# Performance work log

Measured on AMD Instinct MI355X. Metric: run time of the kernel, lower is better.

Reference implementation:

```python
import jax, jax.numpy as jnp
import numpy as np

D = 768
LAYERS = 4
LN_EPS = 1e-5


def _layer_norm(h, g, b):
    m = jnp.mean(h, axis=-1, keepdims=True)
    v = jnp.var(h, axis=-1, keepdims=True)
    return (h - m) * jax.lax.rsqrt(v + LN_EPS) * g + b


def _encode(ids, emb, ln_g, ln_b, w1, b1, w2, b2):
    # ids: [N, F] int, emb: [F, V, D] stacked embedding tables
    h = emb[0][ids[:, 0]]
    for i in range(1, emb.shape[0]):
        h = h + emb[i][ids[:, i]]
    h = _layer_norm(h, ln_g, ln_b)
    h = jax.nn.gelu(jnp.dot(h, w1) + b1)
    return jnp.dot(h, w2) + b2


def setup_inputs() -> dict:
    key = jax.random.key(0)
    ks = jax.random.split(key, 24)
    N, E = 50000, 100000
    s = 0.02
    inp = {
        "x": jax.random.randint(ks[0], (N, 9), 0, 128),
        "edge_attr": jax.random.randint(ks[1], (E, 3), 0, 8),
        "edge_index": jax.random.randint(ks[2], (2, E), 0, N),
        # AtomEncoder params
        "atom_emb": jax.random.normal(ks[3], (9, 128, D), jnp.float32) * s,
        "atom_ln_g": jnp.ones((D,), jnp.float32),
        "atom_ln_b": jnp.zeros((D,), jnp.float32),
        "atom_w1": jax.random.normal(ks[4], (D, D), jnp.float32) * s,
        "atom_b1": jnp.zeros((D,), jnp.float32),
        "atom_w2": jax.random.normal(ks[5], (D, D), jnp.float32) * s,
        "atom_b2": jnp.zeros((D,), jnp.float32),
        # BondEncoder params
        "bond_emb": jax.random.normal(ks[6], (3, 8, D), jnp.float32) * s,
        "bond_ln_g": jnp.ones((D,), jnp.float32),
        "bond_ln_b": jnp.zeros((D,), jnp.float32),
        "bond_w1": jax.random.normal(ks[7], (D, D), jnp.float32) * s,
        "bond_b1": jnp.zeros((D,), jnp.float32),
        "bond_w2": jax.random.normal(ks[8], (D, D), jnp.float32) * s,
        "bond_b2": jnp.zeros((D,), jnp.float32),
        # Per-layer GINEConv MLPs + LayerNorms (stacked over layers)
        "conv_w1": jax.random.normal(ks[9], (LAYERS, D, D), jnp.float32) * s,
        "conv_b1": jnp.zeros((LAYERS, D), jnp.float32),
        "conv_w2": jax.random.normal(ks[10], (LAYERS, D, D), jnp.float32) * s,
        "conv_b2": jnp.zeros((LAYERS, D), jnp.float32),
        "ln_g": jnp.ones((LAYERS, D), jnp.float32),
        "ln_b": jnp.zeros((LAYERS, D), jnp.float32),
    }
    return inp


def reference(x, edge_attr, edge_index,
              atom_emb, atom_ln_g, atom_ln_b, atom_w1, atom_b1, atom_w2, atom_b2,
              bond_emb, bond_ln_g, bond_ln_b, bond_w1, bond_b1, bond_w2, bond_b2,
              conv_w1, conv_b1, conv_w2, conv_b2, ln_g, ln_b):
    N = x.shape[0]
    src, dst = edge_index[0], edge_index[1]
    h = _encode(x, atom_emb, atom_ln_g, atom_ln_b, atom_w1, atom_b1, atom_w2, atom_b2)
    e = _encode(edge_attr, bond_emb, bond_ln_g, bond_ln_b, bond_w1, bond_b1, bond_w2, bond_b2)
    for l in range(LAYERS):
        h_in = h
        # GINEConv (eps=0): out = MLP(x + sum_{j in N(i)} relu(x_j + e_ij))
        msg = jax.nn.relu(h[src] + e)                       # [E, D] gather + edge-add + relu
        agg = jax.ops.segment_sum(msg, dst, num_segments=N)  # scatter-add to nodes
        z = h + agg
        z = jnp.dot(jax.nn.relu(jnp.dot(z, conv_w1[l]) + conv_b1[l]), conv_w2[l]) + conv_b2[l]
        # gelu -> dropout (identity at eval) -> residual LayerNorm
        h = _layer_norm(jax.nn.gelu(z) + h_in, ln_g[l], ln_b[l])
    return h
```

## Files before the change

kernel.cpp:

```cpp
#include <hip/hip_runtime.h>


#define DM 768
#define NLAYERS 4
#define CHUNK 50048

typedef _Float16 f16;
typedef __attribute__((ext_vector_type(8))) _Float16 f16x8;
typedef __attribute__((ext_vector_type(4))) _Float16 f16x4;
typedef __attribute__((ext_vector_type(4))) float f32x4;

__device__ __forceinline__ float gelu_f(float x) {
    float x3 = x * x * x;
    return 0.5f * x * (1.0f + tanhf(0.7978845608028654f * (x + 0.044715f * x3)));
}
__device__ __forceinline__ void async16(const void* g, void* l) {
    __builtin_amdgcn_global_load_lds((const __attribute__((address_space(1))) void*)g,
                                     (__attribute__((address_space(3))) void*)l,
                                     16, 0, 0);
}

__device__ __forceinline__ int xcd_swizzle(int b, int nb) {
    int xcd = b & 7;
    int pos = b >> 3;
    int q = nb >> 3, r = nb & 7;
    int base = (xcd < r) ? xcd * (q + 1) : r * (q + 1) + (xcd - r) * q;
    return base + pos;
}

__device__ __forceinline__ void block_reduce2(float& s1, float& s2, float* sm) {
    #pragma unroll
    for (int off = 32; off > 0; off >>= 1) {
        s1 += __shfl_down(s1, off);
        s2 += __shfl_down(s2, off);
    }
    int lane = threadIdx.x & 63, wid = threadIdx.x >> 6;
    if (lane == 0) { sm[wid * 2] = s1; sm[wid * 2 + 1] = s2; }
    __syncthreads();
    s1 = sm[0] + sm[2] + sm[4] + sm[6];
    s2 = sm[1] + sm[3] + sm[5] + sm[7];
}

__global__ __launch_bounds__(256) void transpose768(
    const float* __restrict__ W, f16* __restrict__ Wt) {
    __shared__ float t[32][33];
    int tx = threadIdx.x, ty = threadIdx.y;
    int c0 = blockIdx.x * 32, r0 = blockIdx.y * 32;
    #pragma unroll
    for (int j = 0; j < 32; j += 8) t[ty + j][tx] = W[(r0 + ty + j) * DM + c0 + tx];
    __syncthreads();
    #pragma unroll
    for (int j = 0; j < 32; j += 8) Wt[(long)(c0 + ty + j) * DM + r0 + tx] = (f16)t[tx][ty + j];
}

__global__ __launch_bounds__(256) void embed_ln_kernel(
    const int* __restrict__ ids, int F, int V,
    const float* __restrict__ emb,
    const float* __restrict__ g, const float* __restrict__ b,
    f16* __restrict__ out) {
    int m = blockIdx.x, tid = threadIdx.x;
    float v[3] = {0.f, 0.f, 0.f};
    for (int f = 0; f < F; ++f) {
        int id = ids[(long)m * F + f];
        const float* row = emb + ((long)f * V + id) * DM;
        v[0] += row[tid];
        v[1] += row[tid + 256];
        v[2] += row[tid + 512];
    }
    float s1 = v[0] + v[1] + v[2];
    float s2 = v[0] * v[0] + v[1] * v[1] + v[2] * v[2];
    __shared__ float sm[8];
    block_reduce2(s1, s2, sm);
    float mean = s1 * (1.f / DM);
    float var = s2 * (1.f / DM) - mean * mean;
    float rstd = rsqrtf(var + 1e-5f);
    #pragma unroll
    for (int q = 0; q < 3; ++q) {
        int d = tid + q * 256;
        out[(long)m * DM + d] = (f16)((v[q] - mean) * rstd * g[d] + b[d]);
    }
}

template <typename OUT>
__global__ __launch_bounds__(256) void gelu_res_ln_kernel(
    const f16* __restrict__ U, const f16* __restrict__ hin,
    const float* __restrict__ g, const float* __restrict__ b,
    OUT* __restrict__ out) {
    int m = blockIdx.x, tid = threadIdx.x;
    float v[3];
    #pragma unroll
    for (int q = 0; q < 3; ++q) {
        int d = tid + q * 256;
        v[q] = gelu_f((float)U[(long)m * DM + d]) + (float)hin[(long)m * DM + d];
    }
    float s1 = v[0] + v[1] + v[2];
    float s2 = v[0] * v[0] + v[1] * v[1] + v[2] * v[2];
    __shared__ float sm[8];
    block_reduce2(s1, s2, sm);
    float mean = s1 * (1.f / DM);
    float var = s2 * (1.f / DM) - mean * mean;
    float rstd = rsqrtf(var + 1e-5f);
    #pragma unroll
    for (int q = 0; q < 3; ++q) {
        int d = tid + q * 256;
        out[(long)m * DM + d] = (OUT)((v[q] - mean) * rstd * g[d] + b[d]);
    }
}

__global__ __launch_bounds__(256) void make_combo_ids(
    int V, int nC, int* __restrict__ ids) {
    int c = blockIdx.x * 256 + threadIdx.x;
    if (c >= nC) return;
    ids[c * 3 + 0] = c / (V * V);
    ids[c * 3 + 1] = (c / V) % V;
    ids[c * 3 + 2] = c % V;
}
__global__ __launch_bounds__(256) void make_key_kernel(
    const int* __restrict__ ea, int E, int V, int* __restrict__ key) {
    int e = blockIdx.x * 256 + threadIdx.x;
    if (e >= E) return;
    key[e] = (ea[e * 3 + 0] * V + ea[e * 3 + 1]) * V + ea[e * 3 + 2];
}

__global__ __launch_bounds__(256) void build_list_kernel(
    const int* __restrict__ ei, int E,
    int* __restrict__ head, int* __restrict__ nxt) {
    int e = blockIdx.x * 256 + threadIdx.x;
    if (e >= E) return;
    int dst = ei[E + e];
    nxt[e] = atomicExch(&head[dst], e);
}

__global__ __launch_bounds__(256) void gather_agg_kernel(
    const int* __restrict__ ei,
    const int* __restrict__ head, const int* __restrict__ nxt,
    const int* __restrict__ key,
    const f16* __restrict__ h, const f16* __restrict__ T,
    f16* __restrict__ z, int N) {
    int node = blockIdx.x * 4 + (threadIdx.x >> 6);
    if (node >= N) return;
    int lane = threadIdx.x & 63;
    int base = lane * 12;

    const f16* hr = h + (long)node * DM + base;
    f16x4 v0 = *(const f16x4*)&hr[0];
    f16x4 v1 = *(const f16x4*)&hr[4];
    f16x4 v2 = *(const f16x4*)&hr[8];
    float acc[12];
    #pragma unroll
    for (int j = 0; j < 4; ++j) {
        acc[j]     = (float)v0[j];
        acc[4 + j] = (float)v1[j];
        acc[8 + j] = (float)v2[j];
    }

    int ecur = head[node];
    while (ecur >= 0) {
        int enext = nxt[ecur];
        int src = ei[ecur];
        int kq = key[ecur];
        const f16* sr = h + (long)src * DM + base;
        const f16* er = T + (long)kq * DM + base;
        f16x4 a0 = *(const f16x4*)&sr[0];
        f16x4 a1 = *(const f16x4*)&sr[4];
        f16x4 a2 = *(const f16x4*)&sr[8];
        f16x4 b0 = *(const f16x4*)&er[0];
        f16x4 b1 = *(const f16x4*)&er[4];
        f16x4 b2 = *(const f16x4*)&er[8];
        #pragma unroll
        for (int j = 0; j < 4; ++j) {
            float m0 = (float)a0[j] + (float)b0[j];
            float m1 = (float)a1[j] + (float)b1[j];
            float m2 = (float)a2[j] + (float)b2[j];
            if (m0 > 0.f) acc[j]     += m0;
            if (m1 > 0.f) acc[4 + j] += m1;
            if (m2 > 0.f) acc[8 + j] += m2;
        }
        ecur = enext;
    }

    f16* zr = z + (long)node * DM + base;
    f16x4 o0, o1, o2;
    #pragma unroll
    for (int j = 0; j < 4; ++j) {
        o0[j] = (f16)acc[j];
        o1[j] = (f16)acc[4 + j];
        o2[j] = (f16)acc[8 + j];
    }
    *(f16x4*)&zr[0] = o0;
    *(f16x4*)&zr[4] = o1;
    *(f16x4*)&zr[8] = o2;
}

#define ACT_NONE 0
#define ACT_RELU 1
#define ACT_GELU 2

template <int ACT>
__global__ __launch_bounds__(256, 2) void gemm768(
    const f16* __restrict__ A,
    const f16* __restrict__ Bt,
    const float* __restrict__ bias,
    f16* __restrict__ C,
    int M) {
    __shared__ f16 As[128 * 32];
    __shared__ f16 Bs[128 * 32];
    int tid = threadIdx.x;
    int lane = tid & 63;
    int wid = tid >> 6;
    int wm = wid >> 1, wn = wid & 1;

    int wg = xcd_swizzle(blockIdx.x, gridDim.x);
    int rt = wg / 6, cb = wg - rt * 6;
    long rowBase = (long)rt * 128;
    const f16* Ab = A + rowBase * DM;
    const f16* Bb = Bt + (long)cb * 128 * DM;

    f32x4 acc[4][4];
    #pragma unroll
    for (int i = 0; i < 4; ++i)
        #pragma unroll
        for (int j = 0; j < 4; ++j) acc[i][j] = (f32x4){0.f, 0.f, 0.f, 0.f};

    int sr = wid * 32;
    int lr = lane >> 2;
    int lc = (((lane & 3) ^ ((lr >> 1) & 3)) * 8);
    int fm = lane & 15;
    int fk = (lane >> 4) * 8;
    int fs = fk ^ (((fm >> 1) & 3) << 3);

    for (int kt = 0; kt < DM / 32; ++kt) {
        int k0 = kt * 32;
        const f16* g0 = Ab + (long)(sr + lr) * DM + k0 + lc;
        async16(g0, &As[sr * 32]);
        async16(g0 + 16 * DM, &As[(sr + 16) * 32]);
        const f16* h0 = Bb + (long)(sr + lr) * DM + k0 + lc;
        async16(h0, &Bs[sr * 32]);
        async16(h0 + 16 * DM, &Bs[(sr + 16) * 32]);
        __syncthreads();

        f16x8 af[4], bfr[4];
        #pragma unroll
        for (int i = 0; i < 4; ++i)
            af[i] = *(const f16x8*)&As[(wm * 64 + i * 16 + fm) * 32 + fs];
        #pragma unroll
        for (int j = 0; j < 4; ++j)
            bfr[j] = *(const f16x8*)&Bs[(wn * 64 + j * 16 + fm) * 32 + fs];
        #pragma unroll
        for (int ci = 0; ci < 4; ++ci)
            #pragma unroll
            for (int ri = 0; ri < 4; ++ri)
                acc[ci][ri] = __builtin_amdgcn_mfma_f32_16x16x32_f16(bfr[ci], af[ri], acc[ci][ri], 0, 0, 0);
        __syncthreads();
    }

    int row0 = (int)rowBase + wm * 64;
    int col0 = cb * 128 + wn * 64;
    float4 bv[4];
    #pragma unroll
    for (int ci = 0; ci < 4; ++ci)
        bv[ci] = *(const float4*)&bias[col0 + ci * 16 + (lane >> 4) * 4];
    #pragma unroll
    for (int ri = 0; ri < 4; ++ri) {
        int row = row0 + ri * 16 + (lane & 15);
        if (row < M) {
            #pragma unroll
            for (int ci = 0; ci < 4; ++ci) {
                int c0 = col0 + ci * 16 + (lane >> 4) * 4;
                f16x4 o;
                #pragma unroll
                for (int r = 0; r < 4; ++r) {
                    float v = acc[ci][ri][r] + (&bv[ci].x)[r];
                    if (ACT == ACT_RELU) v = v > 0.f ? v : 0.f;
                    if (ACT == ACT_GELU) v = gelu_f(v);
                    o[r] = (f16)v;
                }
                *(f16x4*)&C[(long)row * DM + c0] = o;
            }
        }
    }
}

extern "C" void kernel_launch(void* const* d_in, const int* in_sizes, int n_in,
                              void* d_out, int out_size, void* d_ws, size_t ws_size,
                              hipStream_t stream) {
    const int* x  = (const int*)d_in[0];
    const int* ea = (const int*)d_in[1];
    const int* ei = (const int*)d_in[2];
    const float* atom_emb  = (const float*)d_in[3];
    const float* atom_ln_g = (const float*)d_in[4];
    const float* atom_ln_b = (const float*)d_in[5];
    const float* atom_w1   = (const float*)d_in[6];
    const float* atom_b1   = (const float*)d_in[7];
    const float* atom_w2   = (const float*)d_in[8];
    const float* atom_b2   = (const float*)d_in[9];
    const float* bond_emb  = (const float*)d_in[10];
    const float* bond_ln_g = (const float*)d_in[11];
    const float* bond_ln_b = (const float*)d_in[12];
    const float* bond_w1   = (const float*)d_in[13];
    const float* bond_b1   = (const float*)d_in[14];
    const float* bond_w2   = (const float*)d_in[15];
    const float* bond_b2   = (const float*)d_in[16];
    const float* conv_w1   = (const float*)d_in[17];
    const float* conv_b1   = (const float*)d_in[18];
    const float* conv_w2   = (const float*)d_in[19];
    const float* conv_b2   = (const float*)d_in[20];
    const float* ln_g      = (const float*)d_in[21];
    const float* ln_b      = (const float*)d_in[22];

    const int N = in_sizes[0] / 9;
    const int E = in_sizes[1] / 3;
    const int V = in_sizes[10] / (3 * DM);
    const int nC = V * V * V;
    const long SZ = (long)DM * DM;

    char* ws = (char*)d_ws;
    size_t off = 0;
    f16* WT  = (f16*)(ws + off); off += ((size_t)12 * SZ * 2 + 4095) & ~(size_t)4095;
    f16* Q   = (f16*)(ws + off); off += ((size_t)CHUNK * DM * 2 + 4095) & ~(size_t)4095;
    f16* h   = (f16*)(ws + off); off += ((size_t)N * DM * 2 + 4095) & ~(size_t)4095;
    f16* T   = (f16*)(ws + off); off += ((size_t)((nC + 127) & ~127) * DM * 2 + 4095) & ~(size_t)4095;
    int* key = (int*)(ws + off); off += ((size_t)E * 4 + 4095) & ~(size_t)4095;
    int* ids3 = (int*)(ws + off); off += ((size_t)nC * 12 + 4095) & ~(size_t)4095;
    f16*   U    = (f16*)d_out;
    int*   head = (int*)((char*)d_out + 120000000);
    int*   nxt  = head + N;

    dim3 tb(32, 8), tg(24, 24);
    transpose768<<<tg, tb, 0, stream>>>(atom_w1, WT + 0 * SZ);
    transpose768<<<tg, tb, 0, stream>>>(atom_w2, WT + 1 * SZ);
    transpose768<<<tg, tb, 0, stream>>>(bond_w1, WT + 2 * SZ);
    transpose768<<<tg, tb, 0, stream>>>(bond_w2, WT + 3 * SZ);
    for (int l = 0; l < NLAYERS; ++l) {
        transpose768<<<tg, tb, 0, stream>>>(conv_w1 + l * SZ, WT + (4 + l) * SZ);
        transpose768<<<tg, tb, 0, stream>>>(conv_w2 + l * SZ, WT + (8 + l) * SZ);
    }

    hipMemsetAsync(head, 0xFF, (size_t)N * 4, stream);
    build_list_kernel<<<(E + 255) / 256, 256, 0, stream>>>(ei, E, head, nxt);
    make_key_kernel<<<(E + 255) / 256, 256, 0, stream>>>(ea, E, V, key);

    int rtN = (N + 127) / 128;
    dim3 gn(6 * rtN);

    embed_ln_kernel<<<N, 256, 0, stream>>>(x, 9, 128, atom_emb, atom_ln_g, atom_ln_b, Q);
    gemm768<ACT_GELU><<<gn, 256, 0, stream>>>(Q, WT + 0 * SZ, atom_b1, U, N);
    gemm768<ACT_NONE><<<gn, 256, 0, stream>>>(U, WT + 1 * SZ, atom_b2, h, N);

    make_combo_ids<<<(nC + 255) / 256, 256, 0, stream>>>(V, nC, ids3);
    embed_ln_kernel<<<nC, 256, 0, stream>>>(ids3, 3, V, bond_emb, bond_ln_g, bond_ln_b, Q);
    dim3 gt(6 * ((nC + 127) / 128));
    gemm768<ACT_GELU><<<gt, 256, 0, stream>>>(Q, WT + 2 * SZ, bond_b1, U, nC);
    gemm768<ACT_NONE><<<gt, 256, 0, stream>>>(U, WT + 3 * SZ, bond_b2, T, nC);

    for (int l = 0; l < NLAYERS; ++l) {
        gather_agg_kernel<<<(N + 3) / 4, 256, 0, stream>>>(ei, head, nxt, key, h, T, Q, N);
        gemm768<ACT_RELU><<<gn, 256, 0, stream>>>(Q, WT + (4 + l) * SZ, conv_b1 + l * DM, U, N);
        gemm768<ACT_NONE><<<gn, 256, 0, stream>>>(U, WT + (8 + l) * SZ, conv_b2 + l * DM, Q, N);
        if (l == NLAYERS - 1) {
            gelu_res_ln_kernel<float><<<N, 256, 0, stream>>>(Q, h, ln_g + l * DM, ln_b + l * DM, (float*)d_out);
        } else {
            gelu_res_ln_kernel<f16><<<N, 256, 0, stream>>>(Q, h, ln_g + l * DM, ln_b + l * DM, h);
        }
    }
}
```

Measured before the change: 1.676 ms.

## Double-buffer GEMM LDS tiles with async prefetch and cheaper GELU tanh

The 768-wide GEMM now uses two LDS buffers per operand. It prefetches the next K-tile with global_load_lds while computing on the current one, and waits with vmcnt so only the older loads must finish. This overlaps global-to-LDS transfer with MFMA work instead of serialising them. It also replaces tanhf in GELU with an exp-based formula. Costs are double the LDS footprint, which may limit occupancy at 2 blocks/CU, plus reliance on manual waitcnt and barrier ordering.

Result: faster. 1.610 ms (-3.9%).

```diff
diff --git a/kernel.cpp b/kernel.cpp
--- a/kernel.cpp
+++ b/kernel.cpp
@@ -11,8 +11,11 @@
 typedef __attribute__((ext_vector_type(4))) float f32x4;
 
 __device__ __forceinline__ float gelu_f(float x) {
-    float x3 = x * x * x;
-    return 0.5f * x * (1.0f + tanhf(0.7978845608028654f * (x + 0.044715f * x3)));
+    float u = 0.7978845608028654f * (x + 0.044715f * x * x * x);
+    float a = __expf(-2.0f * fabsf(u));
+    float t = (1.0f - a) / (1.0f + a);
+    t = copysignf(t, u);
+    return 0.5f * x * (1.0f + t);
 }
 __device__ __forceinline__ void async16(const void* g, void* l) {
     __builtin_amdgcn_global_load_lds((const __attribute__((address_space(1))) void*)g,
@@ -203,8 +206,8 @@
     const float* __restrict__ bias,
     f16* __restrict__ C,
     int M) {
-    __shared__ f16 As[128 * 32];
-    __shared__ f16 Bs[128 * 32];
+    __shared__ f16 As[2][128 * 32];
+    __shared__ f16 Bs[2][128 * 32];
     int tid = threadIdx.x;
     int lane = tid & 63;
     int wid = tid >> 6;
@@ -229,29 +232,43 @@
     int fk = (lane >> 4) * 8;
     int fs = fk ^ (((fm >> 1) & 3) << 3);
 
+    const f16* ap = Ab + (long)(sr + lr) * DM + lc;
+    const f16* bp = Bb + (long)(sr + lr) * DM + lc;
+
+    async16(ap, &As[0][sr * 32]);
+    async16(ap + 16 * DM, &As[0][(sr + 16) * 32]);
+    async16(bp, &Bs[0][sr * 32]);
+    async16(bp + 16 * DM, &Bs[0][(sr + 16) * 32]);
+
+    #pragma unroll 2
     for (int kt = 0; kt < DM / 32; ++kt) {
-        int k0 = kt * 32;
-        const f16* g0 = Ab + (long)(sr + lr) * DM + k0 + lc;
-        async16(g0, &As[sr * 32]);
-        async16(g0 + 16 * DM, &As[(sr + 16) * 32]);
-        const f16* h0 = Bb + (long)(sr + lr) * DM + k0 + lc;
-        async16(h0, &Bs[sr * 32]);
-        async16(h0 + 16 * DM, &Bs[(sr + 16) * 32]);
-        __syncthreads();
+        int cur = kt & 1;
+        if (kt + 1 < DM / 32) {
+            int k0 = (kt + 1) * 32;
+            async16(ap + k0, &As[cur ^ 1][sr * 32]);
+            async16(ap + k0 + 16 * DM, &As[cur ^ 1][(sr + 16) * 32]);
+            async16(bp + k0, &Bs[cur ^ 1][sr * 32]);
+            async16(bp + k0 + 16 * DM, &Bs[cur ^ 1][(sr + 16) * 32]);
+            asm volatile("s_waitcnt vmcnt(4)" ::: "memory");
+        } else {
+            asm volatile("s_waitcnt vmcnt(0)" ::: "memory");
+        }
+        __builtin_amdgcn_s_barrier();
 
         f16x8 af[4], bfr[4];
         #pragma unroll
         for (int i = 0; i < 4; ++i)
-            af[i] = *(const f16x8*)&As[(wm * 64 + i * 16 + fm) * 32 + fs];
+            af[i] = *(const f16x8*)&As[cur][(wm * 64 + i * 16 + fm) * 32 + fs];
         #pragma unroll
         for (int j = 0; j < 4; ++j)
-            bfr[j] = *(const f16x8*)&Bs[(wn * 64 + j * 16 + fm) * 32 + fs];
+            bfr[j] = *(const f16x8*)&Bs[cur][(wn * 64 + j * 16 + fm) * 32 + fs];
         #pragma unroll
         for (int ci = 0; ci < 4; ++ci)
             #pragma unroll
             for (int ri = 0; ri < 4; ++ri)
                 acc[ci][ri] = __builtin_amdgcn_mfma_f32_16x16x32_f16(bfr[ci], af[ri], acc[ci][ri], 0, 0, 0);
-        __syncthreads();
+        __builtin_amdgcn_s_barrier();
+        asm volatile("" ::: "memory");
     }
 
     int row0 = (int)rowBase + wm * 64;
```

## Double GEMM K-tile to 64 with new LDS swizzle and fast-exp GELU

Applied to the files above, without the earlier changes.

The 768-wide GEMM now stages 64-wide K tiles in LDS instead of 32-wide ones. This halves the number of load/barrier iterations and issues two MFMA passes per iteration. The LDS XOR swizzle is redone for the 64-column layout to avoid bank conflicts. Separately, tanh in GELU is replaced by an exp-based formula using __expf, which is cheaper but slightly less precise. The larger tile doubles LDS use per block, which could reduce occupancy.

After: 1.549 ms. -7.6%, faster.

```diff
diff --git a/kernel.cpp b/kernel.cpp
--- a/kernel.cpp
+++ b/kernel.cpp
@@ -11,8 +11,11 @@
 typedef __attribute__((ext_vector_type(4))) float f32x4;
 
 __device__ __forceinline__ float gelu_f(float x) {
-    float x3 = x * x * x;
-    return 0.5f * x * (1.0f + tanhf(0.7978845608028654f * (x + 0.044715f * x3)));
+    float u = 0.7978845608028654f * (x + 0.044715f * x * x * x);
+    float a = __expf(-2.0f * fabsf(u));
+    float t = (1.0f - a) / (1.0f + a);
+    t = copysignf(t, u);
+    return 0.5f * x * (1.0f + t);
 }
 __device__ __forceinline__ void async16(const void* g, void* l) {
     __builtin_amdgcn_global_load_lds((const __attribute__((address_space(1))) void*)g,
@@ -203,8 +206,8 @@
     const float* __restrict__ bias,
     f16* __restrict__ C,
     int M) {
-    __shared__ f16 As[128 * 32];
-    __shared__ f16 Bs[128 * 32];
+    __shared__ f16 As[128 * 64];
+    __shared__ f16 Bs[128 * 64];
     int tid = threadIdx.x;
     int lane = tid & 63;
     int wid = tid >> 6;
@@ -223,34 +226,49 @@
         for (int j = 0; j < 4; ++j) acc[i][j] = (f32x4){0.f, 0.f, 0.f, 0.f};
 
     int sr = wid * 32;
-    int lr = lane >> 2;
-    int lc = (((lane & 3) ^ ((lr >> 1) & 3)) * 8);
+    int srow = lane >> 3;
+    int sslot = lane & 7;
+    int scol = ((sslot ^ srow) * 8);
+    const f16* gA = Ab + (long)(sr + srow) * DM + scol;
+    const f16* gB = Bb + (long)(sr + srow) * DM + scol;
+
     int fm = lane & 15;
-    int fk = (lane >> 4) * 8;
-    int fs = fk ^ (((fm >> 1) & 3) << 3);
-
-    for (int kt = 0; kt < DM / 32; ++kt) {
-        int k0 = kt * 32;
-        const f16* g0 = Ab + (long)(sr + lr) * DM + k0 + lc;
-        async16(g0, &As[sr * 32]);
-        async16(g0 + 16 * DM, &As[(sr + 16) * 32]);
-        const f16* h0 = Bb + (long)(sr + lr) * DM + k0 + lc;
-        async16(h0, &Bs[sr * 32]);
-        async16(h0 + 16 * DM, &Bs[(sr + 16) * 32]);
+    int fq = lane >> 4;
+    int rs0 = ((fq ^ (fm & 7)) * 8);
+    int rs1 = (((4 + fq) ^ (fm & 7)) * 8);
+
+    for (int kt = 0; kt < DM / 64; ++kt) {
+        int k0 = kt * 64;
+        #pragma unroll
+        for (int j = 0; j < 4; ++j) {
+            async16(gA + k0 + j * 8 * DM, &As[(sr + j * 8) * 64]);
+            async16(gB + k0 + j * 8 * DM, &Bs[(sr + j * 8) * 64]);
+        }
         __syncthreads();
 
-        f16x8 af[4], bfr[4];
-        #pragma unroll
-        for (int i = 0; i < 4; ++i)
-            af[i] = *(const f16x8*)&As[(wm * 64 + i * 16 + fm) * 32 + fs];
-        #pragma unroll
-        for (int j = 0; j < 4; ++j)
-            bfr[j] = *(const f16x8*)&Bs[(wn * 64 + j * 16 + fm) * 32 + fs];
+        f16x8 af0[4], bf0[4], af1[4], bf1[4];
+        #pragma unroll
+        for (int i = 0; i < 4; ++i) {
+            int ra = (wm * 64 + i * 16 + fm) * 64;
+            af0[i] = *(const f16x8*)&As[ra + rs0];
+            af1[i] = *(const f16x8*)&As[ra + rs1];
+        }
+        #pragma unroll
+        for (int j = 0; j < 4; ++j) {
+            int rb = (wn * 64 + j * 16 + fm) * 64;
+            bf0[j] = *(const f16x8*)&Bs[rb + rs0];
+            bf1[j] = *(const f16x8*)&Bs[rb + rs1];
+        }
         #pragma unroll
         for (int ci = 0; ci < 4; ++ci)
             #pragma unroll
             for (int ri = 0; ri < 4; ++ri)
-                acc[ci][ri] = __builtin_amdgcn_mfma_f32_16x16x32_f16(bfr[ci], af[ri], acc[ci][ri], 0, 0, 0);
+                acc[ci][ri] = __builtin_amdgcn_mfma_f32_16x16x32_f16(bf0[ci], af0[ri], acc[ci][ri], 0, 0, 0);
+        #pragma unroll
+        for (int ci = 0; ci < 4; ++ci)
+            #pragma unroll
+            for (int ri = 0; ri < 4; ++ri)
+                acc[ci][ri] = __builtin_amdgcn_mfma_f32_16x16x32_f16(bf1[ci], af1[ri], acc[ci][ri], 0, 0, 0);
         __syncthreads();
     }
 
```
